# Kernel tuning notes

Measured on AMD Instinct MI355X. Metric: run time of the kernel, lower is better.

The kernel has to match this reference:

```python
import jax, jax.numpy as jnp
import numpy as np

J = 116  # ROI count; c_in = 4*J = 464


def setup_inputs() -> dict:
    key = jax.random.key(0)
    ks = jax.random.split(key, 8)
    B = 131072
    F = jax.random.normal(ks[0], (B, 2, J), dtype=jnp.float32)
    S = jax.random.normal(ks[1], (B, 2, J), dtype=jnp.float32)
    def lin(k, fan_in, fan_out):
        bound = 1.0 / np.sqrt(fan_in)
        kw, kb = jax.random.split(k)
        W = jax.random.uniform(kw, (fan_in, fan_out), jnp.float32, -bound, bound)
        b = jax.random.uniform(kb, (fan_out,), jnp.float32, -bound, bound)
        return W, b
    W1, b1 = lin(ks[2], 4 * J, 64)
    W2, b2 = lin(ks[3], 64, 32)
    W3, b3 = lin(ks[4], 32, 2)
    return {"F": F, "S": S, "W1": W1, "b1": b1, "W2": W2, "b2": b2, "W3": W3, "b3": b3}


def reference(F, S, W1, b1, W2, b2, W3, b3):
    # einsum('bkj,bij->bjki') then mean over (k,i) factors into mean_k(F)*mean_i(S)
    # per (b,j): mean_{k,i} F[b,k,j]*S[b,i,j] = mean_k F[b,k,j] * mean_i S[b,i,j]
    g = jax.nn.sigmoid(jnp.mean(F, axis=1) * jnp.mean(S, axis=1))  # (b, j)
    g = g[:, None, :]                                              # broadcast over the 2 channels
    Fg = F * g
    Sg = S * g
    feat = jnp.concatenate((Fg, Sg), axis=1).reshape(F.shape[0], -1)  # (b, 4*J)
    h = jax.nn.relu(feat @ W1 + b1)
    h = jax.nn.relu(h @ W2 + b2)
    logits = h @ W3 + b3
    return jax.nn.softmax(logits, axis=1)
```

## Files before the change

### kernel.cpp

```cpp
#include <hip/hip_runtime.h>
#include <stdint.h>


typedef float    f4    __attribute__((ext_vector_type(4)));
typedef float    f32x4 __attribute__((ext_vector_type(4)));
typedef _Float16 h8    __attribute__((ext_vector_type(8)));

#define NSTEP 15

__global__ void prep_w1(const float* __restrict__ W1, _Float16* __restrict__ Wsp) {
  const int e  = blockIdx.x * 256 + threadIdx.x;
  const int t  = e >> 11;
  const int r  = e & 2047;
  const int n  = r & 63;
  const int kk = r >> 6;
  const int h  = kk >> 3;
  const int ee = kk & 7;
  const int s  = ee & 1;
  const int jp = ee >> 1;
  const int fam = h >> 1;
  const int j  = 8 * t + 4 * (h & 1) + jp;
  const int ko = 232 * fam + 116 * s + j;
  const float v = (j < 116) ? W1[ko * 64 + n] : 0.f;
  Wsp[t * 2048 + n * 32 + kk] = (_Float16)v;
}

__global__ __launch_bounds__(128, 2) void mricls_main(
    const float* __restrict__ F, const float* __restrict__ S,
    const float* __restrict__ b1, const float* __restrict__ W2,
    const float* __restrict__ b2, const float* __restrict__ W3,
    const float* __restrict__ b3, const _Float16* __restrict__ Wsp,
    float* __restrict__ out) {
  __shared__ __align__(16) union {
    struct { char f[29696]; char s[29696]; } buf;
    float h1[32][68];
  } U;
  __shared__ __align__(16) float W2s[64][32];
  __shared__ __align__(16) float W3s[32][2];
  __shared__ __align__(16) float b1s[64];
  __shared__ __align__(16) float b2s[32];
  __shared__ float b3s[2];

  const int tid = threadIdx.x;
  const int l   = tid & 63;
  const int w   = tid >> 6;
  const int ml  = l & 15;
  const int h   = l >> 4;

  {
    const char* gsrc = ((w == 0) ? (const char*)F : (const char*)S)
                       + (size_t)blockIdx.x * 29696 + l * 16;
    char* ldst = (w == 0) ? U.buf.f : U.buf.s;
#pragma unroll
    for (int g = 0; g < 29; ++g)
      __builtin_amdgcn_global_load_lds(gsrc + g * 1024, ldst + g * 1024, 16, 0, 0);
  }

  {
    const f4* W2v = (const f4*)W2;
    f4* W2sv = (f4*)W2s;
#pragma unroll
    for (int i = 0; i < 4; ++i) W2sv[tid + 128 * i] = W2v[tid + 128 * i];
    if (tid < 16) ((f4*)W3s)[tid] = ((const f4*)W3)[tid];
    if (tid < 16) ((f4*)b1s)[tid] = ((const f4*)b1)[tid];
    if (tid < 8)  ((f4*)b2s)[tid] = ((const f4*)b2)[tid];
    if (tid < 2)  b3s[tid] = b3[tid];
  }

  const char* bb = (const char*)Wsp + ml * 64 + h * 16;
  h8 bq[2][4];
#pragma unroll
  for (int nt = 0; nt < 4; ++nt) bq[0][nt] = *(const h8*)(bb + nt * 1024);

  asm volatile("s_waitcnt vmcnt(0)" ::: "memory");
  __syncthreads();

  const int r  = w * 16 + ml;
  const int fam = h >> 1;
  const char* xb = (fam ? U.buf.s : U.buf.f) + r * 928 + (h & 1) * 16;
  const char* yb = (fam ? U.buf.f : U.buf.s) + r * 928 + (h & 1) * 16;

  f32x4 acc[4];
#pragma unroll
  for (int nt = 0; nt < 4; ++nt) acc[nt] = (f32x4){0.f, 0.f, 0.f, 0.f};

#pragma unroll
  for (int t = 0; t < NSTEP; ++t) {
    if (t + 1 < NSTEP) {
#pragma unroll
      for (int nt = 0; nt < 4; ++nt)
        bq[(t + 1) & 1][nt] = *(const h8*)(bb + (t + 1) * 4096 + nt * 1024);
    }
    const f4 x0 = *(const f4*)(xb + t * 32);
    const f4 x1 = *(const f4*)(xb + t * 32 + 464);
    const f4 y0 = *(const f4*)(yb + t * 32);
    const f4 y1 = *(const f4*)(yb + t * 32 + 464);
    h8 a;
#pragma unroll
    for (int jp = 0; jp < 4; ++jp) {
      const float u = x0[jp] + x1[jp];
      const float v = y0[jp] + y1[jp];
      const float g = 1.f / (1.f + __expf(-0.25f * u * v));
      a[2 * jp]     = (_Float16)(x0[jp] * g);
      a[2 * jp + 1] = (_Float16)(x1[jp] * g);
    }
#pragma unroll
    for (int nt = 0; nt < 4; ++nt)
      acc[nt] = __builtin_amdgcn_mfma_f32_16x16x32_f16(a, bq[t & 1][nt], acc[nt], 0, 0, 0);
  }

  __syncthreads();

#pragma unroll
  for (int nt = 0; nt < 4; ++nt) {
    const int n = nt * 16 + ml;
    const float bias = b1s[n];
#pragma unroll
    for (int rr = 0; rr < 4; ++rr) {
      const int mm = w * 16 + h * 4 + rr;
      U.h1[mm][n] = fmaxf(acc[nt][rr] + bias, 0.f);
    }
  }

  const int m2 = tid >> 2;
  const int q  = tid & 3;
  float acc2[8];
#pragma unroll
  for (int e = 0; e < 8; ++e) acc2[e] = b2s[q * 8 + e];
#pragma unroll 8
  for (int k = 0; k < 64; ++k) {
    const float hk = U.h1[m2][k];
    const f4 w0 = *(const f4*)&W2s[k][q * 8];
    const f4 w1 = *(const f4*)&W2s[k][q * 8 + 4];
    acc2[0] = fmaf(hk, w0[0], acc2[0]);
    acc2[1] = fmaf(hk, w0[1], acc2[1]);
    acc2[2] = fmaf(hk, w0[2], acc2[2]);
    acc2[3] = fmaf(hk, w0[3], acc2[3]);
    acc2[4] = fmaf(hk, w1[0], acc2[4]);
    acc2[5] = fmaf(hk, w1[1], acc2[5]);
    acc2[6] = fmaf(hk, w1[2], acc2[6]);
    acc2[7] = fmaf(hk, w1[3], acc2[7]);
  }
  float p0 = 0.f, p1 = 0.f;
#pragma unroll
  for (int e = 0; e < 8; ++e) {
    const float hv = fmaxf(acc2[e], 0.f);
    p0 = fmaf(hv, W3s[q * 8 + e][0], p0);
    p1 = fmaf(hv, W3s[q * 8 + e][1], p1);
  }
  p0 += __shfl_xor(p0, 1); p0 += __shfl_xor(p0, 2);
  p1 += __shfl_xor(p1, 1); p1 += __shfl_xor(p1, 2);
  if (q == 0) {
    const float l0 = p0 + b3s[0], l1 = p1 + b3s[1];
    const float mx = fmaxf(l0, l1);
    const float e0 = __expf(l0 - mx), e1 = __expf(l1 - mx);
    const float inv = 1.f / (e0 + e1);
    float2 o = make_float2(e0 * inv, e1 * inv);
    *(float2*)(out + ((long)blockIdx.x * 32 + m2) * 2) = o;
  }
}

extern "C" void kernel_launch(void* const* d_in, const int* in_sizes, int n_in,
                              void* d_out, int out_size, void* d_ws, size_t ws_size,
                              hipStream_t stream) {
  const float* F  = (const float*)d_in[0];
  const float* S  = (const float*)d_in[1];
  const float* W1 = (const float*)d_in[2];
  const float* b1 = (const float*)d_in[3];
  const float* W2 = (const float*)d_in[4];
  const float* b2 = (const float*)d_in[5];
  const float* W3 = (const float*)d_in[6];
  const float* b3 = (const float*)d_in[7];
  _Float16* Wsp = (_Float16*)d_ws;
  float* out = (float*)d_out;
  const int B = in_sizes[0] / 232;

  prep_w1<<<dim3(120), dim3(256), 0, stream>>>(W1, Wsp);
  mricls_main<<<dim3(B / 32), dim3(128), 0, stream>>>(F, S, b1, W2, b2, W3, b3,
                                                      (const _Float16*)Wsp, out);
}
```

Before: 301.4 us.

## Make blocks persistent over 16 row tiles with double-buffered register-prefetch staging

```diff
diff --git a/kernel.cpp b/kernel.cpp
--- a/kernel.cpp
+++ b/kernel.cpp
@@ -5,8 +5,11 @@
 typedef float    f4    __attribute__((ext_vector_type(4)));
 typedef float    f32x4 __attribute__((ext_vector_type(4)));
 typedef _Float16 h8    __attribute__((ext_vector_type(8)));
+typedef int      i4    __attribute__((ext_vector_type(4)));
 
 #define NSTEP 15
+#define TPB   16
+#define BUFB  19200
 
 __global__ void prep_w1(const float* __restrict__ W1, _Float16* __restrict__ Wsp) {
   const int e  = blockIdx.x * 256 + threadIdx.x;
@@ -25,16 +28,18 @@
   Wsp[t * 2048 + n * 32 + kk] = (_Float16)v;
 }
 
-__global__ __launch_bounds__(128, 2) void mricls_main(
+#define BL(dst, addr, imm)                                                  \
+  asm volatile("global_load_dwordx4 %0, %1, off offset:" #imm               \
+               : "=v"(dst) : "v"(addr));
+
+__global__ __launch_bounds__(256, 2) void mricls_main(
     const float* __restrict__ F, const float* __restrict__ S,
     const float* __restrict__ b1, const float* __restrict__ W2,
     const float* __restrict__ b2, const float* __restrict__ W3,
     const float* __restrict__ b3, const _Float16* __restrict__ Wsp,
     float* __restrict__ out) {
-  __shared__ __align__(16) union {
-    struct { char f[29696]; char s[29696]; } buf;
-    float h1[32][68];
-  } U;
+  __shared__ __align__(16) char  bufs[2 * BUFB];
+  __shared__ __align__(16) float h1s[16][68];
   __shared__ __align__(16) float W2s[64][32];
   __shared__ __align__(16) float W3s[32][2];
   __shared__ __align__(16) float b1s[64];
@@ -48,115 +53,143 @@
   const int h   = l >> 4;
 
   {
-    const char* gsrc = ((w == 0) ? (const char*)F : (const char*)S)
-                       + (size_t)blockIdx.x * 29696 + l * 16;
-    char* ldst = (w == 0) ? U.buf.f : U.buf.s;
-#pragma unroll
-    for (int g = 0; g < 29; ++g)
-      __builtin_amdgcn_global_load_lds(gsrc + g * 1024, ldst + g * 1024, 16, 0, 0);
-  }
-
-  {
     const f4* W2v = (const f4*)W2;
     f4* W2sv = (f4*)W2s;
 #pragma unroll
-    for (int i = 0; i < 4; ++i) W2sv[tid + 128 * i] = W2v[tid + 128 * i];
+    for (int i = 0; i < 2; ++i) W2sv[tid + 256 * i] = W2v[tid + 256 * i];
     if (tid < 16) ((f4*)W3s)[tid] = ((const f4*)W3)[tid];
     if (tid < 16) ((f4*)b1s)[tid] = ((const f4*)b1)[tid];
     if (tid < 8)  ((f4*)b2s)[tid] = ((const f4*)b2)[tid];
     if (tid < 2)  b3s[tid] = b3[tid];
   }
-
-  const char* bb = (const char*)Wsp + ml * 64 + h * 16;
-  h8 bq[2][4];
-#pragma unroll
-  for (int nt = 0; nt < 4; ++nt) bq[0][nt] = *(const h8*)(bb + nt * 1024);
-
-  asm volatile("s_waitcnt vmcnt(0)" ::: "memory");
+  if (tid < 64) {
+    const int buf = tid >> 5, off16 = (tid >> 4) & 1, rr = tid & 15;
+    *(f4*)(bufs + buf * BUFB + 14 * 1280 + rr * 80 + 16 + off16 * 32) =
+        (f4){0.f, 0.f, 0.f, 0.f};
+  }
+
+  h8 bB[NSTEP];
+  {
+    const char* bb = (const char*)Wsp + (w * 16 + ml) * 64 + h * 16;
+#pragma unroll
+    for (int t = 0; t < NSTEP; ++t) bB[t] = *(const h8*)(bb + t * 4096);
+  }
+
+  const int srow = tid >> 4;
+  const int c    = tid & 15;
+  const float* fc  = F + ((long)blockIdx.x * 256 + srow) * 232 + 4 * c;
+  const float* sc  = S + ((long)blockIdx.x * 256 + srow) * 232 + 4 * c;
+  const float* fc2 = fc + ((c <= 12) ? 64 : 0);
+  const float* sc2 = sc + ((c <= 12) ? 64 : 0);
+
+#define STAGE_QUAD(bufW, q, f0, f1, s0, s1)                                    \
+  {                                                                            \
+    char* wb = (bufW) + ((q) >> 1) * 1280 + srow * 80 + ((q) & 1) * 16;        \
+    h8 fa, sa;                                                                 \
+    _Pragma("unroll")                                                          \
+    for (int jp = 0; jp < 4; ++jp) {                                           \
+      const float u  = f0[jp] + f1[jp];                                        \
+      const float vv = s0[jp] + s1[jp];                                        \
+      const float g  = 1.f / (1.f + __expf(-0.25f * u * vv));                  \
+      fa[2 * jp]     = (_Float16)(f0[jp] * g);                                 \
+      fa[2 * jp + 1] = (_Float16)(f1[jp] * g);                                 \
+      sa[2 * jp]     = (_Float16)(s0[jp] * g);                                 \
+      sa[2 * jp + 1] = (_Float16)(s1[jp] * g);                                 \
+    }                                                                          \
+    *(h8*)(wb)      = fa;                                                      \
+    *(h8*)(wb + 32) = sa;                                                      \
+  }
+
+  {
+    i4 rA, rB, rC, rD, rE, rF_, rG, rH;
+    BL(rA, fc, 0) BL(rB, fc, 464) BL(rC, sc, 0) BL(rD, sc, 464)
+    BL(rE, fc2, 0) BL(rF_, fc2, 464) BL(rG, sc2, 0) BL(rH, sc2, 464)
+    asm volatile("s_waitcnt vmcnt(0)" ::: "memory");
+    __builtin_amdgcn_sched_barrier(0);
+    const f4 f0 = __builtin_bit_cast(f4, rA), f1 = __builtin_bit_cast(f4, rB);
+    const f4 s0 = __builtin_bit_cast(f4, rC), s1 = __builtin_bit_cast(f4, rD);
+    STAGE_QUAD(bufs, c, f0, f1, s0, s1)
+    if (c <= 12) {
+      const f4 g0 = __builtin_bit_cast(f4, rE), g1 = __builtin_bit_cast(f4, rF_);
+      const f4 t0 = __builtin_bit_cast(f4, rG), t1 = __builtin_bit_cast(f4, rH);
+      STAGE_QUAD(bufs, c + 16, g0, g1, t0, t1)
+    }
+  }
   __syncthreads();
 
-  const int r  = w * 16 + ml;
-  const int fam = h >> 1;
-  const char* xb = (fam ? U.buf.s : U.buf.f) + r * 928 + (h & 1) * 16;
-  const char* yb = (fam ? U.buf.f : U.buf.s) + r * 928 + (h & 1) * 16;
-
-  f32x4 acc[4];
-#pragma unroll
-  for (int nt = 0; nt < 4; ++nt) acc[nt] = (f32x4){0.f, 0.f, 0.f, 0.f};
-
-#pragma unroll
-  for (int t = 0; t < NSTEP; ++t) {
-    if (t + 1 < NSTEP) {
-#pragma unroll
-      for (int nt = 0; nt < 4; ++nt)
-        bq[(t + 1) & 1][nt] = *(const h8*)(bb + (t + 1) * 4096 + nt * 1024);
-    }
-    const f4 x0 = *(const f4*)(xb + t * 32);
-    const f4 x1 = *(const f4*)(xb + t * 32 + 464);
-    const f4 y0 = *(const f4*)(yb + t * 32);
-    const f4 y1 = *(const f4*)(yb + t * 32 + 464);
-    h8 a;
-#pragma unroll
-    for (int jp = 0; jp < 4; ++jp) {
-      const float u = x0[jp] + x1[jp];
-      const float v = y0[jp] + y1[jp];
-      const float g = 1.f / (1.f + __expf(-0.25f * u * v));
-      a[2 * jp]     = (_Float16)(x0[jp] * g);
-      a[2 * jp + 1] = (_Float16)(x1[jp] * g);
-    }
-#pragma unroll
-    for (int nt = 0; nt < 4; ++nt)
-      acc[nt] = __builtin_amdgcn_mfma_f32_16x16x32_f16(a, bq[t & 1][nt], acc[nt], 0, 0, 0);
-  }
-
-  __syncthreads();
-
-#pragma unroll
-  for (int nt = 0; nt < 4; ++nt) {
-    const int n = nt * 16 + ml;
-    const float bias = b1s[n];
-#pragma unroll
-    for (int rr = 0; rr < 4; ++rr) {
-      const int mm = w * 16 + h * 4 + rr;
-      U.h1[mm][n] = fmaxf(acc[nt][rr] + bias, 0.f);
-    }
-  }
-
-  const int m2 = tid >> 2;
-  const int q  = tid & 3;
-  float acc2[8];
-#pragma unroll
-  for (int e = 0; e < 8; ++e) acc2[e] = b2s[q * 8 + e];
+  const int aoff = ml * 80 + h * 16;
+
+#pragma unroll 2
+  for (int i = 0; i < TPB; ++i) {
+    i4 rA, rB, rC, rD, rE, rF_, rG, rH;
+    if (i + 1 < TPB) {
+      const float* nfc  = fc  + (i + 1) * 3712;
+      const float* nsc  = sc  + (i + 1) * 3712;
+      const float* nfc2 = fc2 + (i + 1) * 3712;
+      const float* nsc2 = sc2 + (i + 1) * 3712;
+      BL(rA, nfc, 0) BL(rB, nfc, 464) BL(rC, nsc, 0) BL(rD, nsc, 464)
+      BL(rE, nfc2, 0) BL(rF_, nfc2, 464) BL(rG, nsc2, 0) BL(rH, nsc2, 464)
+    }
+
+    const char* bufR = bufs + (i & 1) * BUFB;
+    f32x4 acc = (f32x4){0.f, 0.f, 0.f, 0.f};
+#pragma unroll
+    for (int t = 0; t < NSTEP; ++t) {
+      const h8 a = *(const h8*)(bufR + t * 1280 + aoff);
+      acc = __builtin_amdgcn_mfma_f32_16x16x32_f16(a, bB[t], acc, 0, 0, 0);
+    }
+
+    {
+      const int n = w * 16 + ml;
+      const float bias = b1s[n];
+#pragma unroll
+      for (int r = 0; r < 4; ++r)
+        h1s[h * 4 + r][n] = fmaxf(acc[r] + bias, 0.f);
+    }
+    __syncthreads();
+
+    {
+      const int mrow = tid >> 4;
+      const int u    = tid & 15;
+      float a0 = b2s[2 * u], a1 = b2s[2 * u + 1];
 #pragma unroll 8
-  for (int k = 0; k < 64; ++k) {
-    const float hk = U.h1[m2][k];
-    const f4 w0 = *(const f4*)&W2s[k][q * 8];
-    const f4 w1 = *(const f4*)&W2s[k][q * 8 + 4];
-    acc2[0] = fmaf(hk, w0[0], acc2[0]);
-    acc2[1] = fmaf(hk, w0[1], acc2[1]);
-    acc2[2] = fmaf(hk, w0[2], acc2[2]);
-    acc2[3] = fmaf(hk, w0[3], acc2[3]);
-    acc2[4] = fmaf(hk, w1[0], acc2[4]);
-    acc2[5] = fmaf(hk, w1[1], acc2[5]);
-    acc2[6] = fmaf(hk, w1[2], acc2[6]);
-    acc2[7] = fmaf(hk, w1[3], acc2[7]);
-  }
-  float p0 = 0.f, p1 = 0.f;
-#pragma unroll
-  for (int e = 0; e < 8; ++e) {
-    const float hv = fmaxf(acc2[e], 0.f);
-    p0 = fmaf(hv, W3s[q * 8 + e][0], p0);
-    p1 = fmaf(hv, W3s[q * 8 + e][1], p1);
-  }
-  p0 += __shfl_xor(p0, 1); p0 += __shfl_xor(p0, 2);
-  p1 += __shfl_xor(p1, 1); p1 += __shfl_xor(p1, 2);
-  if (q == 0) {
-    const float l0 = p0 + b3s[0], l1 = p1 + b3s[1];
-    const float mx = fmaxf(l0, l1);
-    const float e0 = __expf(l0 - mx), e1 = __expf(l1 - mx);
-    const float inv = 1.f / (e0 + e1);
-    float2 o = make_float2(e0 * inv, e1 * inv);
-    *(float2*)(out + ((long)blockIdx.x * 32 + m2) * 2) = o;
+      for (int k = 0; k < 64; ++k) {
+        const float hk = h1s[mrow][k];
+        const float2 w2 = *(const float2*)&W2s[k][2 * u];
+        a0 = fmaf(hk, w2.x, a0);
+        a1 = fmaf(hk, w2.y, a1);
+      }
+      const float hv0 = fmaxf(a0, 0.f), hv1 = fmaxf(a1, 0.f);
+      float p0 = hv0 * W3s[2 * u][0] + hv1 * W3s[2 * u + 1][0];
+      float p1 = hv0 * W3s[2 * u][1] + hv1 * W3s[2 * u + 1][1];
+      p0 += __shfl_xor(p0, 1); p0 += __shfl_xor(p0, 2);
+      p0 += __shfl_xor(p0, 4); p0 += __shfl_xor(p0, 8);
+      p1 += __shfl_xor(p1, 1); p1 += __shfl_xor(p1, 2);
+      p1 += __shfl_xor(p1, 4); p1 += __shfl_xor(p1, 8);
+      if (u == 0) {
+        const float l0 = p0 + b3s[0], l1 = p1 + b3s[1];
+        const float mx = fmaxf(l0, l1);
+        const float e0 = __expf(l0 - mx), e1 = __expf(l1 - mx);
+        const float inv = 1.f / (e0 + e1);
+        *(float2*)(out + ((long)blockIdx.x * 256 + i * 16 + mrow) * 2) =
+            make_float2(e0 * inv, e1 * inv);
+      }
+    }
+
+    if (i + 1 < TPB) {
+      asm volatile("s_waitcnt vmcnt(0)" ::: "memory");
+      __builtin_amdgcn_sched_barrier(0);
+      char* bufW = bufs + ((i + 1) & 1) * BUFB;
+      const f4 f0 = __builtin_bit_cast(f4, rA), f1 = __builtin_bit_cast(f4, rB);
+      const f4 s0 = __builtin_bit_cast(f4, rC), s1 = __builtin_bit_cast(f4, rD);
+      STAGE_QUAD(bufW, c, f0, f1, s0, s1)
+      if (c <= 12) {
+        const f4 g0 = __builtin_bit_cast(f4, rE), g1 = __builtin_bit_cast(f4, rF_);
+        const f4 t0 = __builtin_bit_cast(f4, rG), t1 = __builtin_bit_cast(f4, rH);
+        STAGE_QUAD(bufW, c + 16, g0, g1, t0, t1)
+      }
+    }
+    __syncthreads();
   }
 }
 
@@ -176,6 +209,6 @@
   const int B = in_sizes[0] / 232;
 
   prep_w1<<<dim3(120), dim3(256), 0, stream>>>(W1, Wsp);
-  mricls_main<<<dim3(B / 32), dim3(128), 0, stream>>>(F, S, b1, W2, b2, W3, b3,
-                                                      (const _Float16*)Wsp, out);
+  mricls_main<<<dim3(B / 256), dim3(256), 0, stream>>>(F, S, b1, W2, b2, W3, b3,
+                                                       (const _Float16*)Wsp, out);
 }
```

Measured after the change: 277.0 us. 1.09x faster.
